# Kernel tuning notes

Hardware: AMD Instinct MI355X
Metric: run time of the kernel (lower is better)

The kernel has to match this reference:

```python
import jax, jax.numpy as jnp
import numpy as np

N = 20000      # nodes
E = 320000     # edges (before self loops)
IN = 128       # in_channels
HID = 256      # hidden_channels
HEADS = 8
C = HID // HEADS  # 32 per-head dim
L = 4          # num_gat_layers
BN_EPS = 1e-5
LN_EPS = 1e-5


def setup_inputs() -> dict:
    key = jax.random.key(0)
    ks = iter(jax.random.split(key, 64))
    def rn(shape, s=0.05):
        return jax.random.normal(next(ks), shape, jnp.float32) * s
    inp = {
        'x': jax.random.normal(next(ks), (N, IN), jnp.float32),
        'edge_index': jax.random.randint(next(ks), (2, E), 0, N),
        # FeatureMLP
        'mlp_w1': rn((IN, HID)), 'mlp_b1': jnp.zeros((HID,), jnp.float32),
        'bn1_g': jnp.ones((HID,), jnp.float32), 'bn1_b': jnp.zeros((HID,), jnp.float32),
        'mlp_w2': rn((HID, HID)), 'mlp_b2': jnp.zeros((HID,), jnp.float32),
        'bn2_g': jnp.ones((HID,), jnp.float32), 'bn2_b': jnp.zeros((HID,), jnp.float32),
        'mlp_w3': rn((HID, HID)), 'mlp_b3': jnp.zeros((HID,), jnp.float32),
        # stacked GATv2 layer params [L, ...]
        'gat_wl': rn((L, HID, HID)), 'gat_bl': jnp.zeros((L, HID), jnp.float32),
        'gat_wr': rn((L, HID, HID)), 'gat_br': jnp.zeros((L, HID), jnp.float32),
        'gat_att': rn((L, HEADS, C)), 'gat_bias': jnp.zeros((L, HID), jnp.float32),
        'ln_g': jnp.ones((L, HID), jnp.float32), 'ln_b': jnp.zeros((L, HID), jnp.float32),
        'head_w1': rn((2 * HID, HID)), 'head_b1': jnp.zeros((HID,), jnp.float32),
        'hbn1_g': jnp.ones((HID,), jnp.float32), 'hbn1_b': jnp.zeros((HID,), jnp.float32),
        'head_w2': rn((HID, HID // 2)), 'head_b2': jnp.zeros((HID // 2,), jnp.float32),
        'hbn2_g': jnp.ones((HID // 2,), jnp.float32), 'hbn2_b': jnp.zeros((HID // 2,), jnp.float32),
        'head_w3': rn((HID // 2, HID // 4)), 'head_b3': jnp.zeros((HID // 4,), jnp.float32),
        'head_w4': rn((HID // 4, 1)), 'head_b4': jnp.zeros((1,), jnp.float32),
    }
    return inp


def _lrelu01(v):
    return jax.nn.leaky_relu(v, 0.1)


def _bn_eval(v, g, b):
    # eval-mode BatchNorm1d with running_mean=0, running_var=1
    return v * (g / jnp.sqrt(1.0 + BN_EPS)) + b


def _layernorm(v, g, b):
    mu = jnp.mean(v, axis=-1, keepdims=True)
    var = jnp.mean((v - mu) ** 2, axis=-1, keepdims=True)
    return (v - mu) / jnp.sqrt(var + LN_EPS) * g + b


def _gatv2(x, src, dst, Wl, bl, Wr, br, att, bias):
    n = x.shape[0]
    xl = (x @ Wl + bl).reshape(n, HEADS, C)   # source transform
    xr = (x @ Wr + br).reshape(n, HEADS, C)   # target transform
    # per-edge attention logits (GATv2): a . LeakyReLU(x_l[src] + x_r[dst])
    e = jax.nn.leaky_relu(xl[src] + xr[dst], 0.2)          # [E, H, C]
    logits = jnp.einsum('ehc,hc->eh', e, att)               # [E, H]
    # segment softmax over destination nodes
    m = jax.ops.segment_max(logits, dst, num_segments=n)    # [N, H]
    a = jnp.exp(logits - m[dst])
    s = jax.ops.segment_sum(a, dst, num_segments=n)
    alpha = a / (s[dst] + 1e-16)                            # [E, H]
    out = jax.ops.segment_sum(xl[src] * alpha[:, :, None], dst, num_segments=n)
    return out.reshape(n, HID) + bias


def _forward(x, mlp_w1, mlp_b1, bn1_g, bn1_b, mlp_w2, mlp_b2, bn2_g, bn2_b,
             mlp_w3, mlp_b3, gat_wl, gat_bl, gat_wr, gat_br, gat_att, gat_bias,
             ln_g, ln_b, head_w1, head_b1, hbn1_g, hbn1_b, head_w2, head_b2,
             hbn2_g, hbn2_b, head_w3, head_b3, head_w4, head_b4, edge_index):
    n = x.shape[0]
    # FeatureMLP (eval: dropout off)
    h = _lrelu01(_bn_eval(x @ mlp_w1 + mlp_b1, bn1_g, bn1_b))
    h = _lrelu01(_bn_eval(h @ mlp_w2 + mlp_b2, bn2_g, bn2_b))
    x_mlp = h @ mlp_w3 + mlp_b3
    # add self loops
    loop = jnp.arange(n)
    src = jnp.concatenate([edge_index[0], loop])
    dst = jnp.concatenate([edge_index[1], loop])
    g = x_mlp
    for i in range(L):
        res = g
        o = _gatv2(g, src, dst, gat_wl[i], gat_bl[i], gat_wr[i], gat_br[i],
                   gat_att[i], gat_bias[i])
        o = _lrelu01(_layernorm(o, ln_g[i], ln_b[i]))
        g = o + res
    xc = jnp.concatenate([x_mlp, g], axis=1)                # [N, 2*HID]
    h = _lrelu01(_bn_eval(xc @ head_w1 + head_b1, hbn1_g, hbn1_b))
    h = _lrelu01(_bn_eval(h @ head_w2 + head_b2, hbn2_g, hbn2_b))
    h = _lrelu01(h @ head_w3 + head_b3)
    return h @ head_w4 + head_b4                            # [N, 1]


def reference(x, edge_index, mlp_w1, mlp_b1, bn1_g, bn1_b, mlp_w2, mlp_b2,
              bn2_g, bn2_b, mlp_w3, mlp_b3, gat_wl, gat_bl, gat_wr, gat_br,
              gat_att, gat_bias, ln_g, ln_b, head_w1, head_b1, hbn1_g, hbn1_b,
              head_w2, head_b2, hbn2_g, hbn2_b, head_w3, head_b3, head_w4, head_b4):
    return _forward(x, mlp_w1, mlp_b1, bn1_g, bn1_b, mlp_w2, mlp_b2, bn2_g,
                    bn2_b, mlp_w3, mlp_b3, gat_wl, gat_bl, gat_wr, gat_br,
                    gat_att, gat_bias, ln_g, ln_b, head_w1, head_b1, hbn1_g,
                    hbn1_b, head_w2, head_b2, hbn2_g, hbn2_b, head_w3, head_b3,
                    head_w4, head_b4, edge_index)
```

## Files before the change

### kernel.cpp

```cpp
#include <hip/hip_runtime.h>
#include <hip/hip_bf16.h>

#define N_NODES 20000
#define E_EDGES 320000
#define E_TOT   (E_EDGES + N_NODES)
#define IN_CH   128
#define HID     256
#define HEADS   8
#define CPH     32

enum { EP_BIAS = 0, EP_BN_LRELU = 1, EP_LRELU = 2 };

typedef _Float16 f16;
typedef f16  f16x2 __attribute__((ext_vector_type(2)));
typedef f16  f16x4 __attribute__((ext_vector_type(4)));
typedef f16  f16x8 __attribute__((ext_vector_type(8)));
typedef float f32x2 __attribute__((ext_vector_type(2)));
typedef float f32x4 __attribute__((ext_vector_type(4)));

__device__ __forceinline__ f16x2 h2max(f16x2 a, f16x2 b) {
#if __has_builtin(__builtin_elementwise_max)
    return __builtin_elementwise_max(a, b);
#else
    f16x2 r; r[0] = a[0] > b[0] ? a[0] : b[0]; r[1] = a[1] > b[1] ? a[1] : b[1]; return r;
#endif
}
__device__ __forceinline__ float hdot2(f16x2 a, f16x2 b, float c) {
#if __has_builtin(__builtin_amdgcn_fdot2)
    return __builtin_amdgcn_fdot2(a, b, c, false);
#else
    return c + (float)a[0] * (float)b[0] + (float)a[1] * (float)b[1];
#endif
}
__device__ __forceinline__ float fexp2(float x) {
#if __has_builtin(__builtin_amdgcn_exp2f)
    return __builtin_amdgcn_exp2f(x);
#else
    return exp2f(x);
#endif
}

__device__ __forceinline__ size_t frag_idx(int row, int col, int KB) {
    int kb = col >> 6, ks = (col >> 5) & 1, q = (col >> 3) & 3, e = col & 7;
    return ((((size_t)(row >> 4) * KB + kb) * 2 + ks) << 9) + (((q << 4) | (row & 15)) << 3) + e;
}

struct WDesc { const float* src; f16* dst; int K; int Nc; int NTOT; int ct0; };
struct WDescs { WDesc d[14]; };

__global__ __launch_bounds__(256)
void wprep_kernel(WDescs ds) {
    WDesc w = ds.d[blockIdx.y];
    int total = w.K * w.Nc;
    int i = blockIdx.x * 256 + threadIdx.x;
    if (i < total) {
        int NT_local = w.Nc >> 4;
        int e  = i & 7;
        int l  = (i >> 3) & 63;
        int r  = i >> 9;
        int ct = r % NT_local;
        int q  = r / NT_local;
        int ks = q & 1;
        int kb = q >> 1;
        int n  = ct * 16 + (l & 15);
        int k  = kb * 64 + ks * 32 + ((l >> 4) << 3) + e;
        size_t di = (((size_t)(kb * 2 + ks) * w.NTOT + w.ct0 + ct) << 9) + (l << 3) + e;
        w.dst[di] = (f16)w.src[(size_t)k * w.Nc + n];
    }
}

__global__ void cvt_frag_kernel(const float* __restrict__ in, f16* __restrict__ out) {
    int i = blockIdx.x * 256 + threadIdx.x;
    if (i < N_NODES * IN_CH) {
        int row = i / IN_CH, col = i - row * IN_CH;
        out[frag_idx(row, col, 2)] = (f16)in[i];
    }
}

template<int NT, int NTOT, int WAVES, int RT, int DOT, int OUTF>
__global__ __launch_bounds__(WAVES * 64)
void gemm_kernel(const f16* __restrict__ A1, int KB1,
                 const f16* __restrict__ A2, int KB2,
                 const f16* __restrict__ Wf,
                 const float* __restrict__ biasA,
                 const float* __restrict__ biasB,
                 const float* __restrict__ bng,
                 const float* __restrict__ bnb,
                 f16* __restrict__ out16A,
                 f16* __restrict__ out16B,
                 f16* __restrict__ dup16,
                 float* __restrict__ out32,
                 const float* __restrict__ dotw,
                 const float* __restrict__ dotb,
                 float* __restrict__ outdot,
                 int NcA, int KBo, int mode)
{
    __shared__ float red[DOT ? 16 : 1][DOT ? 65 : 1];
    const int tid  = threadIdx.x;
    const int wave = tid >> 6;
    const int lane = tid & 63;
    const int quad = lane >> 4;
    const int rb0 = blockIdx.x * RT;
    const int KBt = KB1 + KB2;

    f32x4 acc[RT][NT];
#pragma unroll
    for (int t = 0; t < RT; ++t)
#pragma unroll
        for (int j = 0; j < NT; ++j) acc[t][j] = (f32x4){0.f, 0.f, 0.f, 0.f};

#pragma unroll 2
    for (int kb = 0; kb < KBt; ++kb) {
#pragma unroll
        for (int ks = 0; ks < 2; ++ks) {
            f16x8 a[RT];
#pragma unroll
            for (int t = 0; t < RT; ++t) {
                const f16* ap = (kb < KB1)
                    ? A1 + (((((size_t)(rb0 + t)) * KB1 + kb) * 2 + ks) << 9) + (lane << 3)
                    : A2 + (((((size_t)(rb0 + t)) * KB2 + (kb - KB1)) * 2 + ks) << 9) + (lane << 3);
                a[t] = *(const f16x8*)ap;
            }
            const f16* bp = Wf + (((size_t)(kb * 2 + ks) * NTOT + wave * NT) << 9) + (lane << 3);
#pragma unroll
            for (int ct = 0; ct < NT; ++ct) {
                f16x8 b = *(const f16x8*)(bp + ((size_t)ct << 9));
#pragma unroll
                for (int t = 0; t < RT; ++t)
                    acc[t][ct] = __builtin_amdgcn_mfma_f32_16x16x32_f16(a[t], b, acc[t][ct], 0, 0, 0);
            }
        }
    }

    const int c0 = lane & 15;
    const int NcB = NTOT * 16 - NcA;
#pragma unroll
    for (int t = 0; t < RT; ++t) {
        const int r0 = (rb0 + t) * 16 + (quad << 2);
#pragma unroll
        for (int ct = 0; ct < NT; ++ct) {
            int col = (wave * NT + ct) * 16 + c0;
            bool isB = col >= NcA;
            int colL = isB ? col - NcA : col;
            float bv = isB ? biasB[colL] : biasA[colL];
            float sc = 1.f, sh = 0.f;
            if (mode == EP_BN_LRELU) {
                sc = bng[col] * rsqrtf(1.f + 1e-5f);
                sh = bnb[col];
            }
#pragma unroll
            for (int reg = 0; reg < 4; ++reg) {
                int row = r0 + reg;
                float v = acc[t][ct][reg] + bv;
                if (mode == EP_BN_LRELU) { v = v * sc + sh; v = v > 0.f ? v : 0.1f * v; }
                else if (mode == EP_LRELU) { v = v > 0.f ? v : 0.1f * v; }
                if (DOT) {
                    red[(quad << 2) + reg][col] = v * dotw[col];
                } else if (OUTF) {
                    size_t idx = frag_idx(row, col, KBo);
                    out16A[idx] = (f16)v;
                    if (dup16) dup16[idx] = (f16)v;
                    if (out32) out32[(size_t)row * NcA + col] = v;
                } else {
                    f16* Cout = isB ? out16B : out16A;
                    int stride = isB ? NcB : NcA;
                    Cout[(size_t)row * stride + colL] = (f16)v;
                }
            }
        }
    }

    if (DOT) {
        __syncthreads();
        if (wave == 0) {
            int r = lane & 15, q = lane >> 4;
            float psum = 0.f;
#pragma unroll
            for (int j = 0; j < 16; ++j) psum += red[r][q * 16 + j];
            psum += __shfl_xor(psum, 16, 64);
            psum += __shfl_xor(psum, 32, 64);
            if (lane < 16) outdot[rb0 * 16 + r] = psum + dotb[0];
        }
    }
}

__global__ void deg_count_kernel(const int* __restrict__ dst, int* __restrict__ cnt) {
    int e = blockIdx.x * 256 + threadIdx.x;
    if (e < E_EDGES) atomicAdd(&cnt[dst[e]], 1);
}
__global__ __launch_bounds__(1024)
void scan_kernel(const int* __restrict__ cnt, int* __restrict__ off) {
    __shared__ int wsum[16];
    __shared__ int wpre[16];
    __shared__ int tot_s;
    __shared__ int carry_s;
    const int tid = threadIdx.x, wv = tid >> 6, ln = tid & 63;
    if (tid == 0) carry_s = 0;
    __syncthreads();
    for (int base = 0; base < N_NODES; base += 1024) {
        int i = base + tid;
        int v = (i < N_NODES) ? cnt[i] + 1 : 0;
        int s = v;
#pragma unroll
        for (int d = 1; d < 64; d <<= 1) { int t = __shfl_up(s, d, 64); if (ln >= d) s += t; }
        if (ln == 63) wsum[wv] = s;
        __syncthreads();
        if (tid < 16) {
            int t = wsum[tid];
            int sc = t;
#pragma unroll
            for (int d = 1; d < 16; d <<= 1) { int u = __shfl_up(sc, d, 16); if (tid >= d) sc += u; }
            wpre[tid] = sc - t;
            if (tid == 15) tot_s = sc;
        }
        __syncthreads();
        if (i < N_NODES) off[i] = carry_s + wpre[wv] + s - v;
        __syncthreads();
        if (tid == 0) carry_s += tot_s;
        __syncthreads();
    }
    if (threadIdx.x == 0) off[N_NODES] = carry_s;
}
__global__ void fill_kernel(const int* __restrict__ src, const int* __restrict__ dst,
                            const int* __restrict__ off, int* __restrict__ cur, int* __restrict__ csr) {
    int i = blockIdx.x * 256 + threadIdx.x;
    if (i < E_EDGES) {
        int d = dst[i];
        int pos = atomicAdd(&cur[d], 1);
        csr[off[d] + pos] = src[i];
    } else {
        int j = i - E_EDGES;
        if (j < N_NODES) csr[off[j + 1] - 1] = j;
    }
}

__global__ __launch_bounds__(256)
void gat_agg_kernel(const f16* __restrict__ xl, const f16* __restrict__ xr,
                    float* __restrict__ g, f16* __restrict__ g16,
                    const int* __restrict__ off, const int* __restrict__ csr,
                    const float* __restrict__ att,
                    const float* __restrict__ bias,
                    const float* __restrict__ lng,
                    const float* __restrict__ lnb)
{
    const int wv = threadIdx.x >> 6;
    const int ln = threadIdx.x & 63;
    const int n  = blockIdx.x * 4 + wv;
    if (n >= N_NODES) return;

    const f16x4* xl4 = (const f16x4*)xl;
    f16x4 xrv = ((const f16x4*)xr)[n * 64 + ln];
    f16x2 xr01; xr01[0] = xrv[0]; xr01[1] = xrv[1];
    f16x2 xr23; xr23[0] = xrv[2]; xr23[1] = xrv[3];
    float4 avf = ((const float4*)att)[ln];
    const float L2E = 1.44269504f;
    f16x2 av01; av01[0] = (f16)(avf.x * L2E); av01[1] = (f16)(avf.y * L2E);
    f16x2 av23; av23[0] = (f16)(avf.z * L2E); av23[1] = (f16)(avf.w * L2E);
    const f16x2 k02 = { (f16)0.2f, (f16)0.2f };

    float s = 0.f, o0 = 0.f, o1 = 0.f, o2 = 0.f, o3 = 0.f;

    auto proc = [&](f16x4 xv) {
        f16x2 x01; x01[0] = xv[0]; x01[1] = xv[1];
        f16x2 x23; x23[0] = xv[2]; x23[1] = xv[3];
        f16x2 v01 = x01 + xr01;
        f16x2 v23 = x23 + xr23;
        f16x2 l01 = h2max(v01, v01 * k02);
        f16x2 l23 = h2max(v23, v23 * k02);
        float pr = hdot2(l01, av01, hdot2(l23, av23, 0.f));
        pr += __shfl_xor(pr, 4, 8);
        pr += __shfl_xor(pr, 2, 8);
        pr += __shfl_xor(pr, 1, 8);
        float e = fexp2(pr);
        s += e;
        o0 = fmaf((float)xv[0], e, o0);
        o1 = fmaf((float)xv[1], e, o1);
        o2 = fmaf((float)xv[2], e, o2);
        o3 = fmaf((float)xv[3], e, o3);
    };

    int p = off[n], end = off[n + 1];
    for (; p + 4 <= end; p += 4) {
        int s0 = csr[p], s1 = csr[p + 1], s2 = csr[p + 2], s3 = csr[p + 3];
        f16x4 r0 = xl4[s0 * 64 + ln];
        f16x4 r1 = xl4[s1 * 64 + ln];
        f16x4 r2 = xl4[s2 * 64 + ln];
        f16x4 r3 = xl4[s3 * 64 + ln];
        proc(r0); proc(r1); proc(r2); proc(r3);
    }
    for (; p < end; ++p) {
        f16x4 r0 = xl4[csr[p] * 64 + ln];
        proc(r0);
    }

    float inv = 1.f / (s + 1e-16f);
    float4 bi = ((const float4*)bias)[ln];
    float y0 = o0 * inv + bi.x;
    float y1 = o1 * inv + bi.y;
    float y2 = o2 * inv + bi.z;
    float y3 = o3 * inv + bi.w;

    float s1 = y0 + y1 + y2 + y3;
    float s2 = y0 * y0 + y1 * y1 + y2 * y2 + y3 * y3;
#pragma unroll
    for (int d = 32; d; d >>= 1) { s1 += __shfl_xor(s1, d, 64); s2 += __shfl_xor(s2, d, 64); }
    float mu  = s1 * (1.f / HID);
    float ex2 = s2 * (1.f / HID);
    float rstd = rsqrtf(ex2 - mu * mu + 1e-5f);
    float4 lg = ((const float4*)lng)[ln];
    float4 lb = ((const float4*)lnb)[ln];
    float nv0 = (y0 - mu) * rstd * lg.x + lb.x; nv0 = nv0 > 0.f ? nv0 : 0.1f * nv0;
    float nv1 = (y1 - mu) * rstd * lg.y + lb.y; nv1 = nv1 > 0.f ? nv1 : 0.1f * nv1;
    float nv2 = (y2 - mu) * rstd * lg.z + lb.z; nv2 = nv2 > 0.f ? nv2 : 0.1f * nv2;
    float nv3 = (y3 - mu) * rstd * lg.w + lb.w; nv3 = nv3 > 0.f ? nv3 : 0.1f * nv3;

    float4 gv = ((const float4*)g)[n * 64 + ln];
    float g0 = nv0 + gv.x, g1 = nv1 + gv.y, g2 = nv2 + gv.z, g3 = nv3 + gv.w;
    ((float4*)g)[n * 64 + ln] = make_float4(g0, g1, g2, g3);
    f16x4 gh; gh[0] = (f16)g0; gh[1] = (f16)g1; gh[2] = (f16)g2; gh[3] = (f16)g3;
    *(f16x4*)&g16[frag_idx(n, 4 * ln, 4)] = gh;
}

static inline size_t align_up(size_t v, size_t a) { return (v + a - 1) & ~(a - 1); }

extern "C" void kernel_launch(void* const* d_in, const int* in_sizes, int n_in,
                              void* d_out, int out_size, void* d_ws, size_t ws_size,
                              hipStream_t stream)
{
    const float* x      = (const float*)d_in[0];
    const int*   ei     = (const int*)d_in[1];
    const float* mlp_w1 = (const float*)d_in[2];
    const float* mlp_b1 = (const float*)d_in[3];
    const float* bn1_g  = (const float*)d_in[4];
    const float* bn1_b  = (const float*)d_in[5];
    const float* mlp_w2 = (const float*)d_in[6];
    const float* mlp_b2 = (const float*)d_in[7];
    const float* bn2_g  = (const float*)d_in[8];
    const float* bn2_b  = (const float*)d_in[9];
    const float* mlp_w3 = (const float*)d_in[10];
    const float* mlp_b3 = (const float*)d_in[11];
    const float* gat_wl = (const float*)d_in[12];
    const float* gat_bl = (const float*)d_in[13];
    const float* gat_wr = (const float*)d_in[14];
    const float* gat_br = (const float*)d_in[15];
    const float* gat_att  = (const float*)d_in[16];
    const float* gat_bias = (const float*)d_in[17];
    const float* ln_g   = (const float*)d_in[18];
    const float* ln_b   = (const float*)d_in[19];
    const float* head_w1 = (const float*)d_in[20];
    const float* head_b1 = (const float*)d_in[21];
    const float* hbn1_g  = (const float*)d_in[22];
    const float* hbn1_b  = (const float*)d_in[23];
    const float* head_w2 = (const float*)d_in[24];
    const float* head_b2 = (const float*)d_in[25];
    const float* hbn2_g  = (const float*)d_in[26];
    const float* hbn2_b  = (const float*)d_in[27];
    const float* head_w3 = (const float*)d_in[28];
    const float* head_b3 = (const float*)d_in[29];
    const float* head_w4 = (const float*)d_in[30];
    const float* head_b4 = (const float*)d_in[31];
    float* out = (float*)d_out;

    char* w = (char*)d_ws;
    size_t p = 0;
    int* off  = (int*)(w + p); p = align_up(p + (N_NODES + 1) * sizeof(int), 64);
    int* fill = (int*)(w + p); p = align_up(p + N_NODES * sizeof(int), 64);
    int* cur  = (int*)(w + p); p = align_up(p + N_NODES * sizeof(int), 64);
    int* csr  = (int*)(w + p); p = align_up(p + E_TOT * sizeof(int), 64);
    float* g32 = (float*)(w + p); p = align_up(p + (size_t)N_NODES * HID * 4, 64);
    auto halloc = [&](size_t elems) {
        f16* q = (f16*)(w + p);
        p = align_up(p + elems * 2, 1024);
        return q;
    };
    f16* x16     = halloc((size_t)N_NODES * IN_CH);
    f16* h1      = halloc((size_t)N_NODES * HID);
    f16* h2      = halloc((size_t)N_NODES * HID);
    f16* x_mlp16 = halloc((size_t)N_NODES * HID);
    f16* g16     = halloc((size_t)N_NODES * HID);
    f16* xl16    = halloc((size_t)N_NODES * HID);
    f16* xr16    = halloc((size_t)N_NODES * HID);
    f16* wt_mlp1 = halloc((size_t)IN_CH * HID);
    f16* wt_mlp2 = halloc((size_t)HID * HID);
    f16* wt_mlp3 = halloc((size_t)HID * HID);
    f16* wt_g[4];
    for (int i = 0; i < 4; ++i) wt_g[i] = halloc((size_t)HID * 2 * HID);
    f16* wt_h1 = halloc((size_t)2 * HID * HID);
    f16* wt_h2 = halloc((size_t)HID * (HID / 2));
    f16* wt_h3 = halloc((size_t)(HID / 2) * (HID / 4));
    (void)ws_size; (void)in_sizes; (void)n_in; (void)out_size;

    const int* e_src = ei;
    const int* e_dst = ei + E_EDGES;

    dim3 blk(256);
    dim3 gM625((N_NODES + 31) / 32);
    dim3 gM1250((N_NODES + 15) / 16);

    WDescs ds;
    ds.d[0]  = { mlp_w1, wt_mlp1, IN_CH, HID, 16, 0 };
    ds.d[1]  = { mlp_w2, wt_mlp2, HID, HID, 16, 0 };
    ds.d[2]  = { mlp_w3, wt_mlp3, HID, HID, 16, 0 };
    for (int i = 0; i < 4; ++i) {
        ds.d[3 + 2 * i] = { gat_wl + (size_t)i * HID * HID, wt_g[i], HID, HID, 32, 0 };
        ds.d[4 + 2 * i] = { gat_wr + (size_t)i * HID * HID, wt_g[i], HID, HID, 32, 16 };
    }
    ds.d[11] = { head_w1, wt_h1, 2 * HID, HID, 16, 0 };
    ds.d[12] = { head_w2, wt_h2, HID, HID / 2, 8, 0 };
    ds.d[13] = { head_w3, wt_h3, HID / 2, HID / 4, 4, 0 };
    {
        dim3 gp((2 * HID * HID + 255) / 256, 14);
        wprep_kernel<<<gp, blk, 0, stream>>>(ds);
    }
    cvt_frag_kernel<<<(N_NODES * IN_CH + 255) / 256, blk, 0, stream>>>(x, x16);

    hipMemsetAsync(fill, 0, (size_t)((char*)cur - (char*)fill) + N_NODES * sizeof(int), stream);
    deg_count_kernel<<<(E_EDGES + 255) / 256, blk, 0, stream>>>(e_dst, fill);
    scan_kernel<<<1, 1024, 0, stream>>>(fill, off);
    fill_kernel<<<(E_TOT + 255) / 256, blk, 0, stream>>>(e_src, e_dst, off, cur, csr);

    gemm_kernel<2, 16, 8, 2, 0, 1><<<gM625, 512, 0, stream>>>(x16, 2, nullptr, 0, wt_mlp1, mlp_b1, mlp_b1,
        bn1_g, bn1_b, h1, nullptr, nullptr, nullptr, nullptr, nullptr, nullptr, HID, 4, EP_BN_LRELU);
    gemm_kernel<2, 16, 8, 2, 0, 1><<<gM625, 512, 0, stream>>>(h1, 4, nullptr, 0, wt_mlp2, mlp_b2, mlp_b2,
        bn2_g, bn2_b, h2, nullptr, nullptr, nullptr, nullptr, nullptr, nullptr, HID, 4, EP_BN_LRELU);
    gemm_kernel<2, 16, 8, 2, 0, 1><<<gM625, 512, 0, stream>>>(h2, 4, nullptr, 0, wt_mlp3, mlp_b3, mlp_b3,
        nullptr, nullptr, x_mlp16, nullptr, g16, g32, nullptr, nullptr, nullptr, HID, 4, EP_BIAS);

    for (int i = 0; i < 4; ++i) {
        gemm_kernel<4, 32, 8, 2, 0, 0><<<gM625, 512, 0, stream>>>(g16, 4, nullptr, 0, wt_g[i],
            gat_bl + i * HID, gat_br + i * HID, nullptr, nullptr,
            xl16, xr16, nullptr, nullptr, nullptr, nullptr, nullptr, HID, 0, EP_BIAS);
        gat_agg_kernel<<<(N_NODES + 3) / 4, blk, 0, stream>>>(xl16, xr16, g32, g16, off, csr,
                                                              gat_att + i * HID, gat_bias + i * HID,
                                                              ln_g + i * HID, ln_b + i * HID);
    }

    gemm_kernel<2, 16, 8, 2, 0, 1><<<gM625, 512, 0, stream>>>(x_mlp16, 4, g16, 4, wt_h1, head_b1, head_b1,
        hbn1_g, hbn1_b, h1, nullptr, nullptr, nullptr, nullptr, nullptr, nullptr, HID, 4, EP_BN_LRELU);
    gemm_kernel<1, 8, 8, 2, 0, 1><<<gM625, 512, 0, stream>>>(h1, 4, nullptr, 0, wt_h2, head_b2, head_b2,
        hbn2_g, hbn2_b, h2, nullptr, nullptr, nullptr, nullptr, nullptr, nullptr, HID / 2, 2, EP_BN_LRELU);
    gemm_kernel<1, 4, 4, 1, 1, 0><<<gM1250, 256, 0, stream>>>(h2, 2, nullptr, 0, wt_h3, head_b3, head_b3,
        nullptr, nullptr, nullptr, nullptr, nullptr, nullptr, head_w4, head_b4, out, HID / 4, 0, EP_LRELU);
}
```

Before: 461.4 us.

## Fuse prep kernels, widen GAT aggregation lanes, single-pass scan, larger GEMM row tiles

Merges weight repacking, input conversion, degree counting and cursor zeroing into one prep kernel, which removes several launches and shrinks the memset. The scan becomes a single pass in which each thread scans 20 elements serially. GAT aggregation now has each half-wave process a different edge using 8-wide f16 loads, combining the halves at the end, to raise memory-level parallelism per wave. GEMM row tiles double from 2 to 4 (fewer, larger blocks), with an added row bound guard because 20000 is not a multiple of 64.

```diff
diff --git a/kernel.cpp b/kernel.cpp
--- a/kernel.cpp
+++ b/kernel.cpp
@@ -48,32 +48,47 @@
 struct WDesc { const float* src; f16* dst; int K; int Nc; int NTOT; int ct0; };
 struct WDescs { WDesc d[14]; };
 
+#define WPREP_BLKS (14 * 512)
+#define CVT_BLKS   ((N_NODES * IN_CH) / 256)
+#define DEG_BLKS   ((E_EDGES + 255) / 256)
+#define ZERO_BLKS  ((N_NODES + 255) / 256)
+#define PREP_BLKS  (WPREP_BLKS + CVT_BLKS + DEG_BLKS + ZERO_BLKS)
+
 __global__ __launch_bounds__(256)
-void wprep_kernel(WDescs ds) {
-    WDesc w = ds.d[blockIdx.y];
-    int total = w.K * w.Nc;
-    int i = blockIdx.x * 256 + threadIdx.x;
-    if (i < total) {
-        int NT_local = w.Nc >> 4;
-        int e  = i & 7;
-        int l  = (i >> 3) & 63;
-        int r  = i >> 9;
-        int ct = r % NT_local;
-        int q  = r / NT_local;
-        int ks = q & 1;
-        int kb = q >> 1;
-        int n  = ct * 16 + (l & 15);
-        int k  = kb * 64 + ks * 32 + ((l >> 4) << 3) + e;
-        size_t di = (((size_t)(kb * 2 + ks) * w.NTOT + w.ct0 + ct) << 9) + (l << 3) + e;
-        w.dst[di] = (f16)w.src[(size_t)k * w.Nc + n];
-    }
-}
-
-__global__ void cvt_frag_kernel(const float* __restrict__ in, f16* __restrict__ out) {
-    int i = blockIdx.x * 256 + threadIdx.x;
-    if (i < N_NODES * IN_CH) {
-        int row = i / IN_CH, col = i - row * IN_CH;
-        out[frag_idx(row, col, 2)] = (f16)in[i];
+void prep_kernel(WDescs ds, const float* __restrict__ x, f16* __restrict__ x16,
+                 const int* __restrict__ dstE, int* __restrict__ cnt, int* __restrict__ cur)
+{
+    const int bx = blockIdx.x;
+    const int tid = threadIdx.x;
+    if (bx < WPREP_BLKS) {
+        WDesc w = ds.d[bx >> 9];
+        int i = ((bx & 511) << 8) + tid;
+        if (i < w.K * w.Nc) {
+            int NT_local = w.Nc >> 4;
+            int e  = i & 7;
+            int l  = (i >> 3) & 63;
+            int r  = i >> 9;
+            int ct = r % NT_local;
+            int q  = r / NT_local;
+            int ks = q & 1;
+            int kb = q >> 1;
+            int n  = ct * 16 + (l & 15);
+            int k  = kb * 64 + ks * 32 + ((l >> 4) << 3) + e;
+            size_t di = (((size_t)(kb * 2 + ks) * w.NTOT + w.ct0 + ct) << 9) + (l << 3) + e;
+            w.dst[di] = (f16)w.src[(size_t)k * w.Nc + n];
+        }
+    } else if (bx < WPREP_BLKS + CVT_BLKS) {
+        int i = (bx - WPREP_BLKS) * 256 + tid;
+        if (i < N_NODES * IN_CH) {
+            int row = i / IN_CH, col = i - row * IN_CH;
+            x16[frag_idx(row, col, 2)] = (f16)x[i];
+        }
+    } else if (bx < WPREP_BLKS + CVT_BLKS + DEG_BLKS) {
+        int e = (bx - WPREP_BLKS - CVT_BLKS) * 256 + tid;
+        if (e < E_EDGES) atomicAdd(&cnt[dstE[e]], 1);
+    } else {
+        int i = (bx - WPREP_BLKS - CVT_BLKS - DEG_BLKS) * 256 + tid;
+        if (i < N_NODES) cur[i] = 0;
     }
 }
 
@@ -156,15 +171,17 @@
                 else if (mode == EP_LRELU) { v = v > 0.f ? v : 0.1f * v; }
                 if (DOT) {
                     red[(quad << 2) + reg][col] = v * dotw[col];
-                } else if (OUTF) {
-                    size_t idx = frag_idx(row, col, KBo);
-                    out16A[idx] = (f16)v;
-                    if (dup16) dup16[idx] = (f16)v;
-                    if (out32) out32[(size_t)row * NcA + col] = v;
-                } else {
-                    f16* Cout = isB ? out16B : out16A;
-                    int stride = isB ? NcB : NcA;
-                    Cout[(size_t)row * stride + colL] = (f16)v;
+                } else if (row < N_NODES) {
+                    if (OUTF) {
+                        size_t idx = frag_idx(row, col, KBo);
+                        out16A[idx] = (f16)v;
+                        if (dup16) dup16[idx] = (f16)v;
+                        if (out32) out32[(size_t)row * NcA + col] = v;
+                    } else {
+                        f16* Cout = isB ? out16B : out16A;
+                        int stride = isB ? NcB : NcA;
+                        Cout[(size_t)row * stride + colL] = (f16)v;
+                    }
                 }
             }
         }
@@ -184,43 +201,37 @@
     }
 }
 
-__global__ void deg_count_kernel(const int* __restrict__ dst, int* __restrict__ cnt) {
-    int e = blockIdx.x * 256 + threadIdx.x;
-    if (e < E_EDGES) atomicAdd(&cnt[dst[e]], 1);
-}
 __global__ __launch_bounds__(1024)
 void scan_kernel(const int* __restrict__ cnt, int* __restrict__ off) {
     __shared__ int wsum[16];
-    __shared__ int wpre[16];
-    __shared__ int tot_s;
-    __shared__ int carry_s;
     const int tid = threadIdx.x, wv = tid >> 6, ln = tid & 63;
-    if (tid == 0) carry_s = 0;
+    const int base = tid * 20;
+    int pre[20];
+    int loc = 0;
+#pragma unroll
+    for (int j = 0; j < 20; ++j) {
+        int i = base + j;
+        int c = (i < N_NODES) ? cnt[i] + 1 : 0;
+        pre[j] = loc;
+        loc += c;
+    }
+    int s = loc;
+#pragma unroll
+    for (int d = 1; d < 64; d <<= 1) { int t = __shfl_up(s, d, 64); if (ln >= d) s += t; }
+    if (ln == 63) wsum[wv] = s;
     __syncthreads();
-    for (int base = 0; base < N_NODES; base += 1024) {
-        int i = base + tid;
-        int v = (i < N_NODES) ? cnt[i] + 1 : 0;
-        int s = v;
-#pragma unroll
-        for (int d = 1; d < 64; d <<= 1) { int t = __shfl_up(s, d, 64); if (ln >= d) s += t; }
-        if (ln == 63) wsum[wv] = s;
-        __syncthreads();
-        if (tid < 16) {
-            int t = wsum[tid];
-            int sc = t;
-#pragma unroll
-            for (int d = 1; d < 16; d <<= 1) { int u = __shfl_up(sc, d, 16); if (tid >= d) sc += u; }
-            wpre[tid] = sc - t;
-            if (tid == 15) tot_s = sc;
-        }
-        __syncthreads();
-        if (i < N_NODES) off[i] = carry_s + wpre[wv] + s - v;
-        __syncthreads();
-        if (tid == 0) carry_s += tot_s;
-        __syncthreads();
-    }
-    if (threadIdx.x == 0) off[N_NODES] = carry_s;
-}
+    int woff = 0;
+#pragma unroll
+    for (int j = 0; j < 16; ++j) if (j < wv) woff += wsum[j];
+    int excl = woff + s - loc;
+#pragma unroll
+    for (int j = 0; j < 20; ++j) {
+        int i = base + j;
+        if (i < N_NODES) off[i] = excl + pre[j];
+    }
+    if (tid == 1023) off[N_NODES] = woff + s;
+}
+
 __global__ void fill_kernel(const int* __restrict__ src, const int* __restrict__ dst,
                             const int* __restrict__ off, int* __restrict__ cur, int* __restrict__ csr) {
     int i = blockIdx.x * 256 + threadIdx.x;
@@ -243,62 +254,95 @@
                     const float* __restrict__ lng,
                     const float* __restrict__ lnb)
 {
-    const int wv = threadIdx.x >> 6;
-    const int ln = threadIdx.x & 63;
-    const int n  = blockIdx.x * 4 + wv;
+    const int wv   = threadIdx.x >> 6;
+    const int ln   = threadIdx.x & 63;
+    const int half = ln >> 5;
+    const int lp   = ln & 31;
+    const int n    = blockIdx.x * 4 + wv;
     if (n >= N_NODES) return;
 
-    const f16x4* xl4 = (const f16x4*)xl;
-    f16x4 xrv = ((const f16x4*)xr)[n * 64 + ln];
-    f16x2 xr01; xr01[0] = xrv[0]; xr01[1] = xrv[1];
-    f16x2 xr23; xr23[0] = xrv[2]; xr23[1] = xrv[3];
-    float4 avf = ((const float4*)att)[ln];
+    const f16x8* xl8 = (const f16x8*)xl;
+    f16x8 xrv = ((const f16x8*)xr)[n * 32 + lp];
+    f16x2 xr0; xr0[0] = xrv[0]; xr0[1] = xrv[1];
+    f16x2 xr1; xr1[0] = xrv[2]; xr1[1] = xrv[3];
+    f16x2 xr2; xr2[0] = xrv[4]; xr2[1] = xrv[5];
+    f16x2 xr3; xr3[0] = xrv[6]; xr3[1] = xrv[7];
+    float4 af0 = ((const float4*)att)[lp * 2];
+    float4 af1 = ((const float4*)att)[lp * 2 + 1];
     const float L2E = 1.44269504f;
-    f16x2 av01; av01[0] = (f16)(avf.x * L2E); av01[1] = (f16)(avf.y * L2E);
-    f16x2 av23; av23[0] = (f16)(avf.z * L2E); av23[1] = (f16)(avf.w * L2E);
+    f16x2 av0; av0[0] = (f16)(af0.x * L2E); av0[1] = (f16)(af0.y * L2E);
+    f16x2 av1; av1[0] = (f16)(af0.z * L2E); av1[1] = (f16)(af0.w * L2E);
+    f16x2 av2; av2[0] = (f16)(af1.x * L2E); av2[1] = (f16)(af1.y * L2E);
+    f16x2 av3; av3[0] = (f16)(af1.z * L2E); av3[1] = (f16)(af1.w * L2E);
     const f16x2 k02 = { (f16)0.2f, (f16)0.2f };
 
-    float s = 0.f, o0 = 0.f, o1 = 0.f, o2 = 0.f, o3 = 0.f;
-
-    auto proc = [&](f16x4 xv) {
-        f16x2 x01; x01[0] = xv[0]; x01[1] = xv[1];
-        f16x2 x23; x23[0] = xv[2]; x23[1] = xv[3];
-        f16x2 v01 = x01 + xr01;
-        f16x2 v23 = x23 + xr23;
-        f16x2 l01 = h2max(v01, v01 * k02);
-        f16x2 l23 = h2max(v23, v23 * k02);
-        float pr = hdot2(l01, av01, hdot2(l23, av23, 0.f));
-        pr += __shfl_xor(pr, 4, 8);
-        pr += __shfl_xor(pr, 2, 8);
-        pr += __shfl_xor(pr, 1, 8);
-        float e = fexp2(pr);
+    float s = 0.f;
+    float o0 = 0.f, o1 = 0.f, o2 = 0.f, o3 = 0.f, o4 = 0.f, o5 = 0.f, o6 = 0.f, o7 = 0.f;
+
+    int p = off[n], end = off[n + 1];
+
+    auto procv = [&](f16x8 xv, bool valid) {
+        f16x2 x0; x0[0] = xv[0]; x0[1] = xv[1];
+        f16x2 x1; x1[0] = xv[2]; x1[1] = xv[3];
+        f16x2 x2; x2[0] = xv[4]; x2[1] = xv[5];
+        f16x2 x3; x3[0] = xv[6]; x3[1] = xv[7];
+        f16x2 v0 = x0 + xr0, v1 = x1 + xr1, v2 = x2 + xr2, v3 = x3 + xr3;
+        v0 = h2max(v0, v0 * k02); v1 = h2max(v1, v1 * k02);
+        v2 = h2max(v2, v2 * k02); v3 = h2max(v3, v3 * k02);
+        float pr = hdot2(v0, av0, hdot2(v1, av1, hdot2(v2, av2, hdot2(v3, av3, 0.f))));
+        pr += __shfl_xor(pr, 1, 64);
+        pr += __shfl_xor(pr, 2, 64);
+        float e = valid ? fexp2(pr) : 0.f;
         s += e;
-        o0 = fmaf((float)xv[0], e, o0);
-        o1 = fmaf((float)xv[1], e, o1);
-        o2 = fmaf((float)xv[2], e, o2);
-        o3 = fmaf((float)xv[3], e, o3);
+        o0 = fmaf((float)xv[0], e, o0); o1 = fmaf((float)xv[1], e, o1);
+        o2 = fmaf((float)xv[2], e, o2); o3 = fmaf((float)xv[3], e, o3);
+        o4 = fmaf((float)xv[4], e, o4); o5 = fmaf((float)xv[5], e, o5);
+        o6 = fmaf((float)xv[6], e, o6); o7 = fmaf((float)xv[7], e, o7);
     };
-
-    int p = off[n], end = off[n + 1];
+    auto proc = [&](int ep) {
+        bool valid = ep < end;
+        int sidx = csr[valid ? ep : end - 1];
+        procv(xl8[(size_t)sidx * 32 + lp], valid);
+    };
+
+    for (; p + 8 <= end; p += 8) {
+        int sA = csr[p +     half];
+        int sB = csr[p + 2 + half];
+        int sC = csr[p + 4 + half];
+        int sD = csr[p + 6 + half];
+        f16x8 rA = xl8[(size_t)sA * 32 + lp];
+        f16x8 rB = xl8[(size_t)sB * 32 + lp];
+        f16x8 rC = xl8[(size_t)sC * 32 + lp];
+        f16x8 rD = xl8[(size_t)sD * 32 + lp];
+        procv(rA, true); procv(rB, true); procv(rC, true); procv(rD, true);
+    }
     for (; p + 4 <= end; p += 4) {
-        int s0 = csr[p], s1 = csr[p + 1], s2 = csr[p + 2], s3 = csr[p + 3];
-        f16x4 r0 = xl4[s0 * 64 + ln];
-        f16x4 r1 = xl4[s1 * 64 + ln];
-        f16x4 r2 = xl4[s2 * 64 + ln];
-        f16x4 r3 = xl4[s3 * 64 + ln];
-        proc(r0); proc(r1); proc(r2); proc(r3);
-    }
-    for (; p < end; ++p) {
-        f16x4 r0 = xl4[csr[p] * 64 + ln];
-        proc(r0);
-    }
+        int sA = csr[p +     half];
+        int sB = csr[p + 2 + half];
+        f16x8 rA = xl8[(size_t)sA * 32 + lp];
+        f16x8 rB = xl8[(size_t)sB * 32 + lp];
+        procv(rA, true); procv(rB, true);
+    }
+    for (; p < end; p += 2) proc(p + half);
+
+    s  += __shfl_xor(s, 32, 64);
+    o0 += __shfl_xor(o0, 32, 64); o1 += __shfl_xor(o1, 32, 64);
+    o2 += __shfl_xor(o2, 32, 64); o3 += __shfl_xor(o3, 32, 64);
+    o4 += __shfl_xor(o4, 32, 64); o5 += __shfl_xor(o5, 32, 64);
+    o6 += __shfl_xor(o6, 32, 64); o7 += __shfl_xor(o7, 32, 64);
+
+    const int lidx = lp * 2 + half;
+    float q0 = half ? o4 : o0;
+    float q1 = half ? o5 : o1;
+    float q2 = half ? o6 : o2;
+    float q3 = half ? o7 : o3;
 
     float inv = 1.f / (s + 1e-16f);
-    float4 bi = ((const float4*)bias)[ln];
-    float y0 = o0 * inv + bi.x;
-    float y1 = o1 * inv + bi.y;
-    float y2 = o2 * inv + bi.z;
-    float y3 = o3 * inv + bi.w;
+    float4 bi = ((const float4*)bias)[lidx];
+    float y0 = q0 * inv + bi.x;
+    float y1 = q1 * inv + bi.y;
+    float y2 = q2 * inv + bi.z;
+    float y3 = q3 * inv + bi.w;
 
     float s1 = y0 + y1 + y2 + y3;
     float s2 = y0 * y0 + y1 * y1 + y2 * y2 + y3 * y3;
@@ -307,18 +351,18 @@
     float mu  = s1 * (1.f / HID);
     float ex2 = s2 * (1.f / HID);
     float rstd = rsqrtf(ex2 - mu * mu + 1e-5f);
-    float4 lg = ((const float4*)lng)[ln];
-    float4 lb = ((const float4*)lnb)[ln];
+    float4 lg = ((const float4*)lng)[lidx];
+    float4 lb = ((const float4*)lnb)[lidx];
     float nv0 = (y0 - mu) * rstd * lg.x + lb.x; nv0 = nv0 > 0.f ? nv0 : 0.1f * nv0;
     float nv1 = (y1 - mu) * rstd * lg.y + lb.y; nv1 = nv1 > 0.f ? nv1 : 0.1f * nv1;
     float nv2 = (y2 - mu) * rstd * lg.z + lb.z; nv2 = nv2 > 0.f ? nv2 : 0.1f * nv2;
     float nv3 = (y3 - mu) * rstd * lg.w + lb.w; nv3 = nv3 > 0.f ? nv3 : 0.1f * nv3;
 
-    float4 gv = ((const float4*)g)[n * 64 + ln];
+    float4 gv = ((const float4*)g)[n * 64 + lidx];
     float g0 = nv0 + gv.x, g1 = nv1 + gv.y, g2 = nv2 + gv.z, g3 = nv3 + gv.w;
-    ((float4*)g)[n * 64 + ln] = make_float4(g0, g1, g2, g3);
+    ((float4*)g)[n * 64 + lidx] = make_float4(g0, g1, g2, g3);
     f16x4 gh; gh[0] = (f16)g0; gh[1] = (f16)g1; gh[2] = (f16)g2; gh[3] = (f16)g3;
-    *(f16x4*)&g16[frag_idx(n, 4 * ln, 4)] = gh;
+    *(f16x4*)&g16[frag_idx(n, 4 * lidx, 4)] = gh;
 }
 
 static inline size_t align_up(size_t v, size_t a) { return (v + a - 1) & ~(a - 1); }
@@ -394,7 +438,7 @@
     const int* e_dst = ei + E_EDGES;
 
     dim3 blk(256);
-    dim3 gM625((N_NODES + 31) / 32);
+    dim3 gM313((N_NODES + 63) / 64);
     dim3 gM1250((N_NODES + 15) / 16);
 
     WDescs ds;
@@ -408,26 +452,21 @@
     ds.d[11] = { head_w1, wt_h1, 2 * HID, HID, 16, 0 };
     ds.d[12] = { head_w2, wt_h2, HID, HID / 2, 8, 0 };
     ds.d[13] = { head_w3, wt_h3, HID / 2, HID / 4, 4, 0 };
-    {
-        dim3 gp((2 * HID * HID + 255) / 256, 14);
-        wprep_kernel<<<gp, blk, 0, stream>>>(ds);
-    }
-    cvt_frag_kernel<<<(N_NODES * IN_CH + 255) / 256, blk, 0, stream>>>(x, x16);
-
-    hipMemsetAsync(fill, 0, (size_t)((char*)cur - (char*)fill) + N_NODES * sizeof(int), stream);
-    deg_count_kernel<<<(E_EDGES + 255) / 256, blk, 0, stream>>>(e_dst, fill);
+
+    hipMemsetAsync(fill, 0, N_NODES * sizeof(int), stream);
+    prep_kernel<<<dim3(PREP_BLKS), blk, 0, stream>>>(ds, x, x16, e_dst, fill, cur);
     scan_kernel<<<1, 1024, 0, stream>>>(fill, off);
     fill_kernel<<<(E_TOT + 255) / 256, blk, 0, stream>>>(e_src, e_dst, off, cur, csr);
 
-    gemm_kernel<2, 16, 8, 2, 0, 1><<<gM625, 512, 0, stream>>>(x16, 2, nullptr, 0, wt_mlp1, mlp_b1, mlp_b1,
+    gemm_kernel<2, 16, 8, 4, 0, 1><<<gM313, 512, 0, stream>>>(x16, 2, nullptr, 0, wt_mlp1, mlp_b1, mlp_b1,
         bn1_g, bn1_b, h1, nullptr, nullptr, nullptr, nullptr, nullptr, nullptr, HID, 4, EP_BN_LRELU);
-    gemm_kernel<2, 16, 8, 2, 0, 1><<<gM625, 512, 0, stream>>>(h1, 4, nullptr, 0, wt_mlp2, mlp_b2, mlp_b2,
+    gemm_kernel<2, 16, 8, 4, 0, 1><<<gM313, 512, 0, stream>>>(h1, 4, nullptr, 0, wt_mlp2, mlp_b2, mlp_b2,
         bn2_g, bn2_b, h2, nullptr, nullptr, nullptr, nullptr, nullptr, nullptr, HID, 4, EP_BN_LRELU);
-    gemm_kernel<2, 16, 8, 2, 0, 1><<<gM625, 512, 0, stream>>>(h2, 4, nullptr, 0, wt_mlp3, mlp_b3, mlp_b3,
+    gemm_kernel<2, 16, 8, 4, 0, 1><<<gM313, 512, 0, stream>>>(h2, 4, nullptr, 0, wt_mlp3, mlp_b3, mlp_b3,
         nullptr, nullptr, x_mlp16, nullptr, g16, g32, nullptr, nullptr, nullptr, HID, 4, EP_BIAS);
 
     for (int i = 0; i < 4; ++i) {
-        gemm_kernel<4, 32, 8, 2, 0, 0><<<gM625, 512, 0, stream>>>(g16, 4, nullptr, 0, wt_g[i],
+        gemm_kernel<4, 32, 8, 4, 0, 0><<<gM313, 512, 0, stream>>>(g16, 4, nullptr, 0, wt_g[i],
             gat_bl + i * HID, gat_br + i * HID, nullptr, nullptr,
             xl16, xr16, nullptr, nullptr, nullptr, nullptr, nullptr, HID, 0, EP_BIAS);
         gat_agg_kernel<<<(N_NODES + 3) / 4, blk, 0, stream>>>(xl16, xr16, g32, g16, off, csr,
@@ -435,9 +474,9 @@
                                                               ln_g + i * HID, ln_b + i * HID);
     }
 
-    gemm_kernel<2, 16, 8, 2, 0, 1><<<gM625, 512, 0, stream>>>(x_mlp16, 4, g16, 4, wt_h1, head_b1, head_b1,
+    gemm_kernel<2, 16, 8, 4, 0, 1><<<gM313, 512, 0, stream>>>(x_mlp16, 4, g16, 4, wt_h1, head_b1, head_b1,
         hbn1_g, hbn1_b, h1, nullptr, nullptr, nullptr, nullptr, nullptr, nullptr, HID, 4, EP_BN_LRELU);
-    gemm_kernel<1, 8, 8, 2, 0, 1><<<gM625, 512, 0, stream>>>(h1, 4, nullptr, 0, wt_h2, head_b2, head_b2,
+    gemm_kernel<1, 8, 8, 4, 0, 1><<<gM313, 512, 0, stream>>>(h1, 4, nullptr, 0, wt_h2, head_b2, head_b2,
         hbn2_g, hbn2_b, h2, nullptr, nullptr, nullptr, nullptr, nullptr, nullptr, HID / 2, 2, EP_BN_LRELU);
     gemm_kernel<1, 4, 4, 1, 1, 0><<<gM1250, 256, 0, stream>>>(h2, 2, nullptr, 0, wt_h3, head_b3, head_b3,
         nullptr, nullptr, nullptr, nullptr, nullptr, nullptr, head_w4, head_b4, out, HID / 4, 0, EP_LRELU);
```

After: 466.7 us. No clear change (+1.1%).
